# Kernel tuning notes

Hardware: AMD Instinct MI355X
Metric: run time of the kernel (lower is better)

## Reference

```python
import jax, jax.numpy as jnp
import numpy as np

B, T, C, H = 8, 2048, 1024, 64

def setup_inputs() -> dict:
    key = jax.random.key(0)
    kx, kk, kq, kv = jax.random.split(key, 4)
    x = jax.random.normal(kx, (B, T, C), dtype=jnp.float32)
    # nn.Linear(n_embed, head_size, bias=False) weights stored as [C, H] (already transposed)
    s = 1.0 / np.sqrt(C)
    Wk = jax.random.normal(kk, (C, H), dtype=jnp.float32) * s
    Wq = jax.random.normal(kq, (C, H), dtype=jnp.float32) * s
    Wv = jax.random.normal(kv, (C, H), dtype=jnp.float32) * s
    return {"x": x, "Wk": Wk, "Wq": Wq, "Wv": Wv}

def reference(x, Wk, Wq, Wv):
    Bq, Tq, Cq = x.shape
    k = jnp.einsum('btc,ch->bth', x, Wk)
    q = jnp.einsum('btc,ch->bth', x, Wq)
    v = jnp.einsum('btc,ch->bth', x, Wv)
    # NOTE: faithful to source, which MULTIPLIES by C**0.5 (not 1/sqrt(head_size))
    wei = jnp.einsum('bth,bsh->bts', q, k) * (Cq ** 0.5)  # [B,T,T]
    causal = jnp.tril(jnp.ones((Tq, Tq), dtype=bool))
    wei = jnp.where(causal, wei, -jnp.inf)
    wei = jax.nn.softmax(wei, axis=-1)
    out = jnp.einsum('bts,bsh->bth', wei, v)  # [B,T,H]
    return out
```

## Files before the change

### kernel.cpp

```cpp
#include <hip/hip_runtime.h>

#define TSEQ 2048
#define CDIM 1024
#define HDIM 64
#define NROW (8 * 2048)

typedef __attribute__((ext_vector_type(8))) short bf16x8;
typedef __attribute__((ext_vector_type(4))) float f32x4;

__device__ __forceinline__ unsigned short f2bf(float f) {
    unsigned int u = __builtin_bit_cast(unsigned int, f);
    u = (u + 0x7FFFu + ((u >> 16) & 1u)) >> 16;
    return (unsigned short)u;
}
__device__ __forceinline__ float bf2f(unsigned short h) {
    unsigned int u = ((unsigned int)h) << 16;
    return __builtin_bit_cast(float, u);
}
__device__ __forceinline__ void split2(float v, unsigned short& h, unsigned short& l) {
    h = f2bf(v);
    l = f2bf(v - bf2f(h));
}
__device__ __forceinline__ f32x4 mfma16(bf16x8 a, bf16x8 b, f32x4 c) {
    return __builtin_amdgcn_mfma_f32_16x16x32_bf16(a, b, c, 0, 0, 0);
}
__device__ __forceinline__ void gload_lds16(const unsigned short* g, unsigned short* l) {
    __builtin_amdgcn_global_load_lds(
        (const __attribute__((address_space(1))) unsigned int*)(g),
        (__attribute__((address_space(3))) unsigned int*)(l), 16, 0, 0);
}
__device__ __forceinline__ void gload_lds16f(const float* g, float* l) {
    __builtin_amdgcn_global_load_lds(
        (const __attribute__((address_space(1))) unsigned int*)(g),
        (__attribute__((address_space(3))) unsigned int*)(l), 16, 0, 0);
}

__global__ __launch_bounds__(256) void w_prep(
    const float* __restrict__ Wk, const float* __restrict__ Wq, const float* __restrict__ Wv,
    unsigned short* __restrict__ wThi, unsigned short* __restrict__ wTlo)
{
    __shared__ float tile[64][65];
    const int mm = blockIdx.x >> 4, kt = blockIdx.x & 15;
    const float* __restrict__ W = (mm == 0) ? Wk : (mm == 1) ? Wq : Wv;
    const int t = threadIdx.x;
    #pragma unroll
    for (int s = 0; s < 4; s++) {
        const int f = t + 256 * s;
        const int r = f >> 4, cq = f & 15;
        const float4 wv = *reinterpret_cast<const float4*>(&W[(long)(kt * 64 + r) * HDIM + 4 * cq]);
        tile[4 * cq + 0][r] = wv.x; tile[4 * cq + 1][r] = wv.y;
        tile[4 * cq + 2][r] = wv.z; tile[4 * cq + 3][r] = wv.w;
    }
    __syncthreads();
    const int n = t >> 2, seg = t & 3;
    unsigned short hi[16], lo[16];
    #pragma unroll
    for (int u = 0; u < 16; u++) split2(tile[n][16 * seg + u], hi[u], lo[u]);
    const long base = (long)(mm * 64 + n) * CDIM + kt * 64 + 16 * seg;
    *reinterpret_cast<uint4*>(&wThi[base + 0]) = *reinterpret_cast<uint4*>(&hi[0]);
    *reinterpret_cast<uint4*>(&wThi[base + 8]) = *reinterpret_cast<uint4*>(&hi[8]);
    *reinterpret_cast<uint4*>(&wTlo[base + 0]) = *reinterpret_cast<uint4*>(&lo[0]);
    *reinterpret_cast<uint4*>(&wTlo[base + 8]) = *reinterpret_cast<uint4*>(&lo[8]);
}

__global__ __launch_bounds__(512, 1) void proj_mfma(
    const float* __restrict__ x,
    const unsigned short* __restrict__ wThi, const unsigned short* __restrict__ wTlo,
    unsigned short* __restrict__ khi, unsigned short* __restrict__ klo,
    unsigned short* __restrict__ qhi, unsigned short* __restrict__ qlo,
    unsigned short* __restrict__ vt)
{
    extern __shared__ __align__(16) unsigned char smem[];
    unsigned short* const wlds = (unsigned short*)smem;
    float* const xlds = (float*)(smem + 2 * 2 * 12288 * 2);

    const int t = threadIdx.x;
    const int lane = t & 63, w = t >> 6;
    const int r15 = lane & 15, g = lane >> 4;
    const int wr = w >> 2, wc = w & 3;
    const int bb8 = blockIdx.x & 7, jj = blockIdx.x >> 3;
    const long rowbase = (long)bb8 * TSEQ + jj * 64;

    const int xrow = t >> 4, xsl = t & 15;
    const long xsrc0 = (rowbase + xrow) * CDIM + ((xsl ^ (xrow & 7)) << 2);
    const int wrow = t >> 3, wsl = t & 7;
    const long wsrc0 = (long)wrow * CDIM + (((wsl ^ (wrow & 7))) << 3);

    f32x4 acc[2][3];
    #pragma unroll
    for (int mt = 0; mt < 2; mt++)
        #pragma unroll
        for (int nt = 0; nt < 3; nt++) acc[mt][nt] = (f32x4){0.f, 0.f, 0.f, 0.f};

    auto stage = [&](int bufn, int kc) {
        float* xd = xlds + bufn * 4096 + t * 4;
        gload_lds16f(&x[xsrc0 + kc], xd);
        gload_lds16f(&x[xsrc0 + 32768 + kc], xd + 2048);
        unsigned short* wd = wlds + bufn * 24576 + t * 8;
        gload_lds16(&wThi[wsrc0 + kc], wd);
        gload_lds16(&wThi[wsrc0 + 65536 + kc], wd + 4096);
        gload_lds16(&wThi[wsrc0 + 131072 + kc], wd + 8192);
        gload_lds16(&wTlo[wsrc0 + kc], wd + 12288);
        gload_lds16(&wTlo[wsrc0 + 65536 + kc], wd + 12288 + 4096);
        gload_lds16(&wTlo[wsrc0 + 131072 + kc], wd + 12288 + 8192);
    };

    stage(0, 0);
    __syncthreads();

    for (int j = 0; j < 16; ++j) {
        const int buf = j & 1;
        if (j < 15) stage(buf ^ 1, (j + 1) * 64);

        const unsigned short* wbase = wlds + buf * 24576;
        const float* xbase = xlds + buf * 4096;

        bf16x8 ah[2][2], al[2][2];
        #pragma unroll
        for (int mt = 0; mt < 2; mt++) {
            const int rx = 32 * wr + 16 * mt + r15;
            const float* xb = xbase + rx * 64;
            const int r7 = rx & 7;
            #pragma unroll
            for (int ks = 0; ks < 2; ks++) {
                const f32x4 a0 = *reinterpret_cast<const f32x4*>(xb + ((8 * ks + ((2 * g) ^ r7)) << 2));
                const f32x4 a1 = *reinterpret_cast<const f32x4*>(xb + ((8 * ks + ((2 * g + 1) ^ r7)) << 2));
                unsigned short h0,h1,h2,h3,h4,h5,h6,h7, l0,l1,l2,l3,l4,l5,l6,l7;
                split2(a0.x, h0, l0); split2(a0.y, h1, l1); split2(a0.z, h2, l2); split2(a0.w, h3, l3);
                split2(a1.x, h4, l4); split2(a1.y, h5, l5); split2(a1.z, h6, l6); split2(a1.w, h7, l7);
                ah[mt][ks] = (bf16x8){(short)h0,(short)h1,(short)h2,(short)h3,(short)h4,(short)h5,(short)h6,(short)h7};
                al[mt][ks] = (bf16x8){(short)l0,(short)l1,(short)l2,(short)l3,(short)l4,(short)l5,(short)l6,(short)l7};
            }
        }
        #pragma unroll
        for (int nt = 0; nt < 3; nt++) {
            const int rw = (3 * wc + nt) * 16 + r15;
            const unsigned short* wh = wbase + rw * 64;
            const unsigned short* wl = wh + 12288;
            const int r7w = rw & 7;
            #pragma unroll
            for (int ks = 0; ks < 2; ks++) {
                const bf16x8 bh = *reinterpret_cast<const bf16x8*>(wh + (((g + 4 * ks) ^ r7w) << 3));
                const bf16x8 bl = *reinterpret_cast<const bf16x8*>(wl + (((g + 4 * ks) ^ r7w) << 3));
                #pragma unroll
                for (int mt = 0; mt < 2; mt++) {
                    acc[mt][nt] = mfma16(ah[mt][ks], bh, acc[mt][nt]);
                    acc[mt][nt] = mfma16(al[mt][ks], bh, acc[mt][nt]);
                    acc[mt][nt] = mfma16(ah[mt][ks], bl, acc[mt][nt]);
                }
            }
        }
        __syncthreads();
    }

    #pragma unroll
    for (int nt = 0; nt < 3; nt++) {
        const int ntg = 3 * wc + nt;
        const int mat = ntg >> 2;
        const int colin = (ntg & 3) * 16 + r15;
        #pragma unroll
        for (int mt = 0; mt < 2; mt++) {
            const int rl = 32 * wr + 16 * mt + 4 * g;
            if (mat == 0) {
                #pragma unroll
                for (int reg = 0; reg < 4; reg++) {
                    unsigned short h, l;
                    split2(acc[mt][nt][reg], h, l);
                    const long idx = (rowbase + rl + reg) * HDIM + colin;
                    khi[idx] = h; klo[idx] = l;
                }
            } else if (mat == 1) {
                #pragma unroll
                for (int reg = 0; reg < 4; reg++) {
                    unsigned short h, l;
                    split2(acc[mt][nt][reg] * 32.0f, h, l);
                    const long idx = (rowbase + rl + reg) * HDIM + colin;
                    qhi[idx] = h; qlo[idx] = l;
                }
            } else {
                ushort4 pk;
                pk.x = f2bf(acc[mt][nt][0]); pk.y = f2bf(acc[mt][nt][1]);
                pk.z = f2bf(acc[mt][nt][2]); pk.w = f2bf(acc[mt][nt][3]);
                const long idx = ((long)bb8 * 64 + colin) * TSEQ + jj * 64 + rl;
                *reinterpret_cast<ushort4*>(&vt[idx]) = pk;
            }
        }
    }
}

__global__ __launch_bounds__(256, 2) void attn_part(
    const unsigned short* __restrict__ khi, const unsigned short* __restrict__ klo,
    const unsigned short* __restrict__ qhi, const unsigned short* __restrict__ qlo,
    const unsigned short* __restrict__ vt,
    float* __restrict__ po, float* __restrict__ pm, float* __restrict__ pl, int nsplit)
{
    __shared__ __align__(16) unsigned short ldsbuf[2][3 * 4096];
    __shared__ __align__(16) unsigned short p_lds4[4][16 * 72];
    const int t = threadIdx.x, w = t >> 6, lane = t & 63;
    const int r15 = lane & 15, g = lane >> 4;
    const int id = blockIdx.x;
    const int b = id & 7;
    const int u = id >> 3;
    const int t5 = u & 31, p = u >> 5;
    int j = (t5 & 1) ? 31 - (t5 >> 1) : (t5 >> 1);
    if (p & 1) j = 31 - j;
    const int n = j + 1;
    const int s = (p * n) / nsplit, e = ((p + 1) * n) / nsplit;
    const int pidx = (b * 32 + j) * nsplit + p;

    if (s >= e) {
        const int rr = t >> 2, cq = (t & 3) * 16;
        if ((t & 3) == 0) { pm[pidx * 64 + rr] = -3e38f; pl[pidx * 64 + rr] = 0.f; }
        const f32x4 z = (f32x4){0.f, 0.f, 0.f, 0.f};
        float* dst = &po[((long)pidx * 64 + rr) * 64 + cq];
        #pragma unroll
        for (int q = 0; q < 4; q++) *reinterpret_cast<f32x4*>(dst + 4 * q) = z;
        return;
    }

    const int row0 = t >> 3;
    const int ce = (((t & 7) ^ (row0 & 7)) << 3);
    const long bkey = (long)b * TSEQ;
    const long vrow = ((long)b * 64 + row0) * TSEQ;
    unsigned short* const lbT = &ldsbuf[0][0];

    auto stage = [&](int cur, int kb) {
        unsigned short* lb = lbT + cur * (3 * 4096) + t * 8;
        const long kgo  = (bkey + (long)kb * 64 + row0) * HDIM + ce;
        const long kgo2 = kgo + 32 * HDIM;
        const long vgo  = vrow + (long)kb * 64 + ce;
        const long vgo2 = vgo + 32L * TSEQ;
        gload_lds16(khi + kgo,  lb);
        gload_lds16(khi + kgo2, lb + 2048);
        gload_lds16(klo + kgo,  lb + 4096);
        gload_lds16(klo + kgo2, lb + 6144);
        gload_lds16(vt  + vgo,  lb + 8192);
        gload_lds16(vt  + vgo2, lb + 10240);
    };

    const long qrow = bkey + (long)j * 64 + 16 * w + r15;
    bf16x8 Qh[2], Ql[2];
    #pragma unroll
    for (int ks = 0; ks < 2; ks++) {
        Qh[ks] = *reinterpret_cast<const bf16x8*>(&qhi[qrow * HDIM + 32 * ks + 8 * g]);
        Ql[ks] = *reinterpret_cast<const bf16x8*>(&qlo[qrow * HDIM + 32 * ks + 8 * g]);
    }

    f32x4 o[4];
    #pragma unroll
    for (int ht = 0; ht < 4; ht++) o[ht] = (f32x4){0.f, 0.f, 0.f, 0.f};
    float m = -3e38f, lsum = 0.f;
    unsigned short* const pw = &p_lds4[w][0];
    const int sw = (r15 & 7) << 4;
    const int c0 = ((16 * g) ^ sw) >> 1;
    const int c1 = ((16 * g + 64) ^ sw) >> 1;

    stage(0, s);
    __syncthreads();

    for (int kb = s; kb < e; ++kb) {
        const int cur = (kb - s) & 1;
        if (kb + 1 < e) stage(cur ^ 1, kb + 1);
        const unsigned short* Kh = lbT + cur * (3 * 4096);
        const unsigned short* Kl = Kh + 4096;
        const unsigned short* Vb = Kh + 8192;
        const bool diag = (kb == j);

        f32x4 sc[4];
        #pragma unroll
        for (int mt = 0; mt < 4; mt++) {
            const bool valid = !diag || (mt <= w);
            f32x4 sv = valid ? (f32x4){0.f, 0.f, 0.f, 0.f}
                             : (f32x4){-1e30f, -1e30f, -1e30f, -1e30f};
            if (valid) {
                const int rb = (16 * mt + r15) * 64;
                const bf16x8 ah0 = *reinterpret_cast<const bf16x8*>(&Kh[rb + c0]);
                const bf16x8 ah1 = *reinterpret_cast<const bf16x8*>(&Kh[rb + c1]);
                const bf16x8 al0 = *reinterpret_cast<const bf16x8*>(&Kl[rb + c0]);
                const bf16x8 al1 = *reinterpret_cast<const bf16x8*>(&Kl[rb + c1]);
                sv = mfma16(ah0, Qh[0], sv);
                sv = mfma16(ah0, Ql[0], sv);
                sv = mfma16(al0, Qh[0], sv);
                sv = mfma16(ah1, Qh[1], sv);
                sv = mfma16(ah1, Ql[1], sv);
                sv = mfma16(al1, Qh[1], sv);
                if (diag && mt == w) {
                    #pragma unroll
                    for (int reg = 0; reg < 4; reg++)
                        if (4 * g + reg > r15) sv[reg] = -1e30f;
                }
            }
            sc[mt] = sv;
        }

        float bml = -3e38f;
        #pragma unroll
        for (int mt = 0; mt < 4; mt++)
            bml = fmaxf(bml, fmaxf(fmaxf(sc[mt][0], sc[mt][1]), fmaxf(sc[mt][2], sc[mt][3])));
        if (!__all(bml - m <= 8.0f)) {
            float bm = fmaxf(bml, __shfl_xor(bml, 16));
            bm = fmaxf(bm, __shfl_xor(bm, 32));
            const float mnew = fmaxf(m, bm);
            const float corr = __expf(m - mnew);
            lsum *= corr;
            #pragma unroll
            for (int ht = 0; ht < 4; ht++) o[ht] *= corr;
            m = mnew;
        }
        #pragma unroll
        for (int mt = 0; mt < 4; mt++) {
            const float p0 = __expf(sc[mt][0] - m);
            const float p1 = __expf(sc[mt][1] - m);
            const float p2 = __expf(sc[mt][2] - m);
            const float p3 = __expf(sc[mt][3] - m);
            lsum += (p0 + p1) + (p2 + p3);
            ushort4 pk;
            pk.x = f2bf(p0); pk.y = f2bf(p1); pk.z = f2bf(p2); pk.w = f2bf(p3);
            *reinterpret_cast<ushort4*>(&pw[r15 * 72 + 16 * mt + 4 * g]) = pk;
        }
        #pragma unroll
        for (int ks = 0; ks < 2; ks++) {
            const bf16x8 pb = *reinterpret_cast<const bf16x8*>(&pw[r15 * 72 + 32 * ks + 8 * g]);
            const int cc = ks ? c1 : c0;
            #pragma unroll
            for (int ht = 0; ht < 4; ht++) {
                const bf16x8 av = *reinterpret_cast<const bf16x8*>(&Vb[(16 * ht + r15) * 64 + cc]);
                o[ht] = mfma16(av, pb, o[ht]);
            }
        }
        __syncthreads();
    }

    lsum += __shfl_xor(lsum, 16);
    lsum += __shfl_xor(lsum, 32);
    if (g == 0) { pm[pidx * 64 + 16 * w + r15] = m; pl[pidx * 64 + 16 * w + r15] = lsum; }
    #pragma unroll
    for (int ht = 0; ht < 4; ht++)
        *reinterpret_cast<f32x4*>(&po[((long)pidx * 64 + 16 * w + r15) * 64 + 16 * ht + 4 * g]) = o[ht];
}

__global__ __launch_bounds__(256) void attn_comb(
    const float* __restrict__ po, const float* __restrict__ pm, const float* __restrict__ pl,
    float* __restrict__ out, int nsplit)
{
    const int t = threadIdx.x;
    const int b = blockIdx.x & 7, j = blockIdx.x >> 3;
    const int r = t >> 2, cq = (t & 3) * 16;
    const int base = (b * 32 + j) * nsplit;

    float M = -3e38f;
    for (int p = 0; p < nsplit; ++p) M = fmaxf(M, pm[(base + p) * 64 + r]);
    float L = 0.f;
    f32x4 acc[4];
    #pragma unroll
    for (int q = 0; q < 4; q++) acc[q] = (f32x4){0.f, 0.f, 0.f, 0.f};
    for (int p = 0; p < nsplit; ++p) {
        const float wp = __expf(pm[(base + p) * 64 + r] - M);
        L += wp * pl[(base + p) * 64 + r];
        const float* src = &po[((long)(base + p) * 64 + r) * 64 + cq];
        #pragma unroll
        for (int q = 0; q < 4; q++) acc[q] += wp * *reinterpret_cast<const f32x4*>(src + 4 * q);
    }
    const float inv = 1.0f / L;
    float* dst = &out[((long)b * TSEQ + j * 64 + r) * HDIM + cq];
    #pragma unroll
    for (int q = 0; q < 4; q++) *reinterpret_cast<f32x4*>(dst + 4 * q) = acc[q] * inv;
}

extern "C" void kernel_launch(void* const* d_in, const int* in_sizes, int n_in,
                              void* d_out, int out_size, void* d_ws, size_t ws_size,
                              hipStream_t stream) {
    const float* x  = (const float*)d_in[0];
    const float* Wk = (const float*)d_in[1];
    const float* Wq = (const float*)d_in[2];
    const float* Wv = (const float*)d_in[3];
    float* outp = (float*)d_out;

    const size_t SZ = (size_t)NROW * HDIM;
    unsigned short* ws   = (unsigned short*)d_ws;
    unsigned short* khi  = ws;
    unsigned short* klo  = ws + 1 * SZ;
    unsigned short* qhi  = ws + 2 * SZ;
    unsigned short* qlo  = ws + 3 * SZ;
    unsigned short* vt   = ws + 4 * SZ;
    unsigned short* wThi = ws + 5 * SZ;
    unsigned short* wTlo = ws + 5 * SZ + 192 * 1024;

    const size_t base_bytes = (5 * SZ + 2 * 192 * 1024) * sizeof(unsigned short);
    int nsplit = 4;
    while (nsplit > 1 && base_bytes + (size_t)nsplit * 4325376 > ws_size) nsplit >>= 1;

    float* po = (float*)((char*)d_ws + base_bytes);
    float* pm = po + (size_t)256 * 64 * 64 * nsplit;
    float* pl = pm + (size_t)256 * 64 * nsplit;

    w_prep<<<48, 256, 0, stream>>>(Wk, Wq, Wv, wThi, wTlo);
    proj_mfma<<<256, 512, 131072, stream>>>(x, wThi, wTlo, khi, klo, qhi, qlo, vt);
    attn_part<<<dim3(256 * nsplit), 256, 0, stream>>>(khi, klo, qhi, qlo, vt, po, pm, pl, nsplit);
    attn_comb<<<256, 256, 0, stream>>>(po, pm, pl, outp, nsplit);
}
```

Measured before the change: 72.96 us.

## Triple-buffer projection K-loop with 32-wide slices and single barrier per step

The projection kernel now splits K into 32-wide slices held in three rotating LDS stages instead of 64-wide slices in two buffers. It waits on outstanding loads with s_waitcnt vmcnt(4) and issues one barrier per iteration, so loads run two stages ahead of the compute. This drops the trailing __syncthreads and cuts dynamic LDS from 128KB to 96KB. The cost is twice as many loop iterations with less MFMA work per barrier, plus a new swizzle layout that must stay correct.

Measured after the change: 74.28 us. About the same (+1.8%).

```diff
diff --git a/kernel.cpp b/kernel.cpp
--- a/kernel.cpp
+++ b/kernel.cpp
@@ -71,9 +71,6 @@
     unsigned short* __restrict__ vt)
 {
     extern __shared__ __align__(16) unsigned char smem[];
-    unsigned short* const wlds = (unsigned short*)smem;
-    float* const xlds = (float*)(smem + 2 * 2 * 12288 * 2);
-
     const int t = threadIdx.x;
     const int lane = t & 63, w = t >> 6;
     const int r15 = lane & 15, g = lane >> 4;
@@ -81,10 +78,17 @@
     const int bb8 = blockIdx.x & 7, jj = blockIdx.x >> 3;
     const long rowbase = (long)bb8 * TSEQ + jj * 64;
 
-    const int xrow = t >> 4, xsl = t & 15;
-    const long xsrc0 = (rowbase + xrow) * CDIM + ((xsl ^ (xrow & 7)) << 2);
-    const int wrow = t >> 3, wsl = t & 7;
-    const long wsrc0 = (long)wrow * CDIM + (((wsl ^ (wrow & 7))) << 3);
+    const unsigned short* wsp[3];
+    #pragma unroll
+    for (int q = 0; q < 3; q++) {
+        const int s = t + 512 * q;
+        const int lo = (s >= 768);
+        const int s7 = s - 768 * lo;
+        const int row = s7 >> 2, sl = s7 & 3;
+        wsp[q] = (lo ? wTlo : wThi) + (long)row * CDIM + ((sl ^ ((row >> 2) & 3)) << 3);
+    }
+    const int xrow_s = t >> 3, xsl_s = t & 7;
+    const float* xsp = x + (rowbase + xrow_s) * CDIM + (((xsl_s ^ (xrow_s & 7))) << 2);
 
     f32x4 acc[2][3];
     #pragma unroll
@@ -92,65 +96,57 @@
         #pragma unroll
         for (int nt = 0; nt < 3; nt++) acc[mt][nt] = (f32x4){0.f, 0.f, 0.f, 0.f};
 
-    auto stage = [&](int bufn, int kc) {
-        float* xd = xlds + bufn * 4096 + t * 4;
-        gload_lds16f(&x[xsrc0 + kc], xd);
-        gload_lds16f(&x[xsrc0 + 32768 + kc], xd + 2048);
-        unsigned short* wd = wlds + bufn * 24576 + t * 8;
-        gload_lds16(&wThi[wsrc0 + kc], wd);
-        gload_lds16(&wThi[wsrc0 + 65536 + kc], wd + 4096);
-        gload_lds16(&wThi[wsrc0 + 131072 + kc], wd + 8192);
-        gload_lds16(&wTlo[wsrc0 + kc], wd + 12288);
-        gload_lds16(&wTlo[wsrc0 + 65536 + kc], wd + 12288 + 4096);
-        gload_lds16(&wTlo[wsrc0 + 131072 + kc], wd + 12288 + 8192);
+    auto stage = [&](int sl, int kc) {
+        unsigned char* base = smem + sl * 32768;
+        #pragma unroll
+        for (int q = 0; q < 3; q++)
+            gload_lds16(wsp[q] + kc, (unsigned short*)(base + (t + 512 * q) * 16));
+        gload_lds16f(xsp + kc, (float*)(base + 24576 + t * 16));
     };
 
-    stage(0, 0);
-    __syncthreads();
-
-    for (int j = 0; j < 16; ++j) {
-        const int buf = j & 1;
-        if (j < 15) stage(buf ^ 1, (j + 1) * 64);
-
-        const unsigned short* wbase = wlds + buf * 24576;
-        const float* xbase = xlds + buf * 4096;
-
-        bf16x8 ah[2][2], al[2][2];
+    auto compute = [&](int sl) {
+        const unsigned short* wb = (const unsigned short*)(smem + sl * 32768);
+        const float* xb = (const float*)(smem + sl * 32768 + 24576);
+        bf16x8 ah[2], al[2];
         #pragma unroll
         for (int mt = 0; mt < 2; mt++) {
             const int rx = 32 * wr + 16 * mt + r15;
-            const float* xb = xbase + rx * 64;
             const int r7 = rx & 7;
-            #pragma unroll
-            for (int ks = 0; ks < 2; ks++) {
-                const f32x4 a0 = *reinterpret_cast<const f32x4*>(xb + ((8 * ks + ((2 * g) ^ r7)) << 2));
-                const f32x4 a1 = *reinterpret_cast<const f32x4*>(xb + ((8 * ks + ((2 * g + 1) ^ r7)) << 2));
-                unsigned short h0,h1,h2,h3,h4,h5,h6,h7, l0,l1,l2,l3,l4,l5,l6,l7;
-                split2(a0.x, h0, l0); split2(a0.y, h1, l1); split2(a0.z, h2, l2); split2(a0.w, h3, l3);
-                split2(a1.x, h4, l4); split2(a1.y, h5, l5); split2(a1.z, h6, l6); split2(a1.w, h7, l7);
-                ah[mt][ks] = (bf16x8){(short)h0,(short)h1,(short)h2,(short)h3,(short)h4,(short)h5,(short)h6,(short)h7};
-                al[mt][ks] = (bf16x8){(short)l0,(short)l1,(short)l2,(short)l3,(short)l4,(short)l5,(short)l6,(short)l7};
-            }
+            const f32x4 a0 = *reinterpret_cast<const f32x4*>(xb + rx * 32 + (((2 * g) ^ r7) << 2));
+            const f32x4 a1 = *reinterpret_cast<const f32x4*>(xb + rx * 32 + (((2 * g + 1) ^ r7) << 2));
+            unsigned short h0,h1,h2,h3,h4,h5,h6,h7, l0,l1,l2,l3,l4,l5,l6,l7;
+            split2(a0.x, h0, l0); split2(a0.y, h1, l1); split2(a0.z, h2, l2); split2(a0.w, h3, l3);
+            split2(a1.x, h4, l4); split2(a1.y, h5, l5); split2(a1.z, h6, l6); split2(a1.w, h7, l7);
+            ah[mt] = (bf16x8){(short)h0,(short)h1,(short)h2,(short)h3,(short)h4,(short)h5,(short)h6,(short)h7};
+            al[mt] = (bf16x8){(short)l0,(short)l1,(short)l2,(short)l3,(short)l4,(short)l5,(short)l6,(short)l7};
         }
         #pragma unroll
         for (int nt = 0; nt < 3; nt++) {
             const int rw = (3 * wc + nt) * 16 + r15;
-            const unsigned short* wh = wbase + rw * 64;
-            const unsigned short* wl = wh + 12288;
-            const int r7w = rw & 7;
+            const int cofs = ((g ^ ((rw >> 2) & 3)) << 3);
+            const bf16x8 bh = *reinterpret_cast<const bf16x8*>(wb + rw * 32 + cofs);
+            const bf16x8 bl = *reinterpret_cast<const bf16x8*>(wb + 6144 + rw * 32 + cofs);
             #pragma unroll
-            for (int ks = 0; ks < 2; ks++) {
-                const bf16x8 bh = *reinterpret_cast<const bf16x8*>(wh + (((g + 4 * ks) ^ r7w) << 3));
-                const bf16x8 bl = *reinterpret_cast<const bf16x8*>(wl + (((g + 4 * ks) ^ r7w) << 3));
-                #pragma unroll
-                for (int mt = 0; mt < 2; mt++) {
-                    acc[mt][nt] = mfma16(ah[mt][ks], bh, acc[mt][nt]);
-                    acc[mt][nt] = mfma16(al[mt][ks], bh, acc[mt][nt]);
-                    acc[mt][nt] = mfma16(ah[mt][ks], bl, acc[mt][nt]);
-                }
+            for (int mt = 0; mt < 2; mt++) {
+                acc[mt][nt] = mfma16(ah[mt], bh, acc[mt][nt]);
+                acc[mt][nt] = mfma16(al[mt], bh, acc[mt][nt]);
+                acc[mt][nt] = mfma16(ah[mt], bl, acc[mt][nt]);
             }
         }
-        __syncthreads();
+    };
+
+    stage(0, 0);
+    stage(1, 32);
+
+    int sA = 0, sB = 1, sC = 2;
+    for (int j = 0; j < 32; ++j) {
+        if (j < 31) { asm volatile("s_waitcnt vmcnt(4)" ::: "memory"); }
+        else        { asm volatile("s_waitcnt vmcnt(0)" ::: "memory"); }
+        __builtin_amdgcn_s_barrier();
+        asm volatile("" ::: "memory");
+        if (j < 30) stage(sC, (j + 2) * 32);
+        compute(sA);
+        const int tmp = sA; sA = sB; sB = sC; sC = tmp;
     }
 
     #pragma unroll
@@ -395,7 +391,7 @@
     float* pl = pm + (size_t)256 * 64 * nsplit;
 
     w_prep<<<48, 256, 0, stream>>>(Wk, Wq, Wv, wThi, wTlo);
-    proj_mfma<<<256, 512, 131072, stream>>>(x, wThi, wTlo, khi, klo, qhi, qlo, vt);
+    proj_mfma<<<256, 512, 98304, stream>>>(x, wThi, wTlo, khi, klo, qhi, qlo, vt);
     attn_part<<<dim3(256 * nsplit), 256, 0, stream>>>(khi, klo, qhi, qlo, vt, po, pm, pl, nsplit);
     attn_comb<<<256, 256, 0, stream>>>(po, pm, pl, outp, nsplit);
 }
```

## Split projection GEMM across output-column halves with smaller blocks and LDS

Applied to the files above, without the earlier changes.

The projection kernel now launches 512 blocks of 256 threads, each computing half of the 192 K/Q/V output columns for a 64-row tile. LDS per block drops from 128 KB to 80 KB and the x tile gets a 16-way XOR swizzle. The aim is better occupancy and load balance across CUs. The cost is that each x tile is loaded and split into bf16 hi/lo twice. The bf16 rounding helper is also switched to the HIP intrinsic __float2bfloat16.

After: 66.73 us. 1.09x faster.

```diff
diff --git a/kernel.cpp b/kernel.cpp
--- a/kernel.cpp
+++ b/kernel.cpp
@@ -1,4 +1,5 @@
 #include <hip/hip_runtime.h>
+#include <hip/hip_bf16.h>
 
 #define TSEQ 2048
 #define CDIM 1024
@@ -9,17 +10,16 @@
 typedef __attribute__((ext_vector_type(4))) float f32x4;
 
 __device__ __forceinline__ unsigned short f2bf(float f) {
-    unsigned int u = __builtin_bit_cast(unsigned int, f);
-    u = (u + 0x7FFFu + ((u >> 16) & 1u)) >> 16;
-    return (unsigned short)u;
+    return __builtin_bit_cast(unsigned short, __float2bfloat16(f));
 }
 __device__ __forceinline__ float bf2f(unsigned short h) {
     unsigned int u = ((unsigned int)h) << 16;
     return __builtin_bit_cast(float, u);
 }
 __device__ __forceinline__ void split2(float v, unsigned short& h, unsigned short& l) {
-    h = f2bf(v);
-    l = f2bf(v - bf2f(h));
+    __hip_bfloat16 bh = __float2bfloat16(v);
+    h = __builtin_bit_cast(unsigned short, bh);
+    l = f2bf(v - __bfloat162float(bh));
 }
 __device__ __forceinline__ f32x4 mfma16(bf16x8 a, bf16x8 b, f32x4 c) {
     return __builtin_amdgcn_mfma_f32_16x16x32_bf16(a, b, c, 0, 0, 0);
@@ -63,7 +63,7 @@
     *reinterpret_cast<uint4*>(&wTlo[base + 8]) = *reinterpret_cast<uint4*>(&lo[8]);
 }
 
-__global__ __launch_bounds__(512, 1) void proj_mfma(
+__global__ __launch_bounds__(256, 4) void proj_mfma(
     const float* __restrict__ x,
     const unsigned short* __restrict__ wThi, const unsigned short* __restrict__ wTlo,
     unsigned short* __restrict__ khi, unsigned short* __restrict__ klo,
@@ -71,20 +71,29 @@
     unsigned short* __restrict__ vt)
 {
     extern __shared__ __align__(16) unsigned char smem[];
-    unsigned short* const wlds = (unsigned short*)smem;
-    float* const xlds = (float*)(smem + 2 * 2 * 12288 * 2);
-
     const int t = threadIdx.x;
     const int lane = t & 63, w = t >> 6;
     const int r15 = lane & 15, g = lane >> 4;
-    const int wr = w >> 2, wc = w & 3;
-    const int bb8 = blockIdx.x & 7, jj = blockIdx.x >> 3;
+    const int wr = w >> 1, wc = w & 1;
+    const int bb8 = blockIdx.x & 7;
+    const int u = blockIdx.x >> 3;
+    const int jj = u >> 1, nh = u & 1;
     const long rowbase = (long)bb8 * TSEQ + jj * 64;
 
-    const int xrow = t >> 4, xsl = t & 15;
-    const long xsrc0 = (rowbase + xrow) * CDIM + ((xsl ^ (xrow & 7)) << 2);
-    const int wrow = t >> 3, wsl = t & 7;
-    const long wsrc0 = (long)wrow * CDIM + (((wsl ^ (wrow & 7))) << 3);
+    long wsrc[3];
+    #pragma unroll
+    for (int q = 0; q < 3; q++) {
+        const int s = t + 256 * q;
+        const int row = s >> 3, gr = s & 7;
+        wsrc[q] = (long)(nh * 96 + row) * CDIM + ((gr ^ (row & 7)) << 3);
+    }
+    long xsrc[4];
+    #pragma unroll
+    for (int q = 0; q < 4; q++) {
+        const int s = t + 256 * q;
+        const int row = s >> 4, gr = s & 15;
+        xsrc[q] = (rowbase + row) * CDIM + ((gr ^ (row & 15)) << 2);
+    }
 
     f32x4 acc[2][3];
     #pragma unroll
@@ -92,39 +101,31 @@
         #pragma unroll
         for (int nt = 0; nt < 3; nt++) acc[mt][nt] = (f32x4){0.f, 0.f, 0.f, 0.f};
 
-    auto stage = [&](int bufn, int kc) {
-        float* xd = xlds + bufn * 4096 + t * 4;
-        gload_lds16f(&x[xsrc0 + kc], xd);
-        gload_lds16f(&x[xsrc0 + 32768 + kc], xd + 2048);
-        unsigned short* wd = wlds + bufn * 24576 + t * 8;
-        gload_lds16(&wThi[wsrc0 + kc], wd);
-        gload_lds16(&wThi[wsrc0 + 65536 + kc], wd + 4096);
-        gload_lds16(&wThi[wsrc0 + 131072 + kc], wd + 8192);
-        gload_lds16(&wTlo[wsrc0 + kc], wd + 12288);
-        gload_lds16(&wTlo[wsrc0 + 65536 + kc], wd + 12288 + 4096);
-        gload_lds16(&wTlo[wsrc0 + 131072 + kc], wd + 12288 + 8192);
+    auto stage = [&](int buf, int kc) {
+        unsigned char* b = smem + buf * 40960;
+        #pragma unroll
+        for (int q = 0; q < 3; q++) {
+            gload_lds16(wThi + wsrc[q] + kc, (unsigned short*)(b + (t + 256 * q) * 16));
+            gload_lds16(wTlo + wsrc[q] + kc, (unsigned short*)(b + 12288 + (t + 256 * q) * 16));
+        }
+        #pragma unroll
+        for (int q = 0; q < 4; q++)
+            gload_lds16f(x + xsrc[q] + kc, (float*)(b + 24576 + (t + 256 * q) * 16));
     };
 
-    stage(0, 0);
-    __syncthreads();
-
-    for (int j = 0; j < 16; ++j) {
-        const int buf = j & 1;
-        if (j < 15) stage(buf ^ 1, (j + 1) * 64);
-
-        const unsigned short* wbase = wlds + buf * 24576;
-        const float* xbase = xlds + buf * 4096;
-
+    auto compute = [&](int buf) {
+        const unsigned short* wb = (const unsigned short*)(smem + buf * 40960);
+        const float* xb = (const float*)(smem + buf * 40960 + 24576);
         bf16x8 ah[2][2], al[2][2];
         #pragma unroll
         for (int mt = 0; mt < 2; mt++) {
             const int rx = 32 * wr + 16 * mt + r15;
-            const float* xb = xbase + rx * 64;
-            const int r7 = rx & 7;
             #pragma unroll
             for (int ks = 0; ks < 2; ks++) {
-                const f32x4 a0 = *reinterpret_cast<const f32x4*>(xb + ((8 * ks + ((2 * g) ^ r7)) << 2));
-                const f32x4 a1 = *reinterpret_cast<const f32x4*>(xb + ((8 * ks + ((2 * g + 1) ^ r7)) << 2));
+                const f32x4 a0 = *reinterpret_cast<const f32x4*>(
+                    xb + rx * 64 + (((8 * ks + 2 * g + 0) ^ r15) << 2));
+                const f32x4 a1 = *reinterpret_cast<const f32x4*>(
+                    xb + rx * 64 + (((8 * ks + 2 * g + 1) ^ r15) << 2));
                 unsigned short h0,h1,h2,h3,h4,h5,h6,h7, l0,l1,l2,l3,l4,l5,l6,l7;
                 split2(a0.x, h0, l0); split2(a0.y, h1, l1); split2(a0.z, h2, l2); split2(a0.w, h3, l3);
                 split2(a1.x, h4, l4); split2(a1.y, h5, l5); split2(a1.z, h6, l6); split2(a1.w, h7, l7);
@@ -135,13 +136,11 @@
         #pragma unroll
         for (int nt = 0; nt < 3; nt++) {
             const int rw = (3 * wc + nt) * 16 + r15;
-            const unsigned short* wh = wbase + rw * 64;
-            const unsigned short* wl = wh + 12288;
-            const int r7w = rw & 7;
             #pragma unroll
             for (int ks = 0; ks < 2; ks++) {
-                const bf16x8 bh = *reinterpret_cast<const bf16x8*>(wh + (((g + 4 * ks) ^ r7w) << 3));
-                const bf16x8 bl = *reinterpret_cast<const bf16x8*>(wl + (((g + 4 * ks) ^ r7w) << 3));
+                const int go = (((4 * ks + g) ^ (rw & 7)) << 3);
+                const bf16x8 bh = *reinterpret_cast<const bf16x8*>(wb + rw * 64 + go);
+                const bf16x8 bl = *reinterpret_cast<const bf16x8*>(wb + 6144 + rw * 64 + go);
                 #pragma unroll
                 for (int mt = 0; mt < 2; mt++) {
                     acc[mt][nt] = mfma16(ah[mt][ks], bh, acc[mt][nt]);
@@ -150,12 +149,20 @@
                 }
             }
         }
+    };
+
+    stage(0, 0);
+    __syncthreads();
+    for (int j = 0; j < 16; ++j) {
+        const int buf = j & 1;
+        if (j < 15) stage(buf ^ 1, (j + 1) * 64);
+        compute(buf);
         __syncthreads();
     }
 
     #pragma unroll
     for (int nt = 0; nt < 3; nt++) {
-        const int ntg = 3 * wc + nt;
+        const int ntg = 6 * nh + 3 * wc + nt;
         const int mat = ntg >> 2;
         const int colin = (ntg & 3) * 16 + r15;
         #pragma unroll
@@ -395,7 +402,7 @@
     float* pl = pm + (size_t)256 * 64 * nsplit;
 
     w_prep<<<48, 256, 0, stream>>>(Wk, Wq, Wv, wThi, wTlo);
-    proj_mfma<<<256, 512, 131072, stream>>>(x, wThi, wTlo, khi, klo, qhi, qlo, vt);
+    proj_mfma<<<512, 256, 81920, stream>>>(x, wThi, wTlo, khi, klo, qhi, qlo, vt);
     attn_part<<<dim3(256 * nsplit), 256, 0, stream>>>(khi, klo, qhi, qlo, vt, po, pm, pl, nsplit);
     attn_comb<<<256, 256, 0, stream>>>(po, pm, pl, outp, nsplit);
 }
```
